# Kernel tuning notes

Hardware: AMD Instinct MI355X
Metric: run time of the kernel (lower is better)

Reference implementation:

```python
import jax, jax.numpy as jnp
import numpy as np

T_DATA = 20000
E_NO = 2000
I_NO = 500
SUB = 12
T_SYN = 200
T_HIST = 100
SB = 3   # syn_basis_no
HB = 3   # hist_basis_no
PB = 3   # prop_basis_no


def setup_inputs() -> dict:
    key = jax.random.key(0)
    ks = jax.random.split(key, 20)
    f32 = jnp.float32
    S_e = (jax.random.uniform(ks[0], (T_DATA, E_NO)) < 0.05).astype(f32)
    S_i = (jax.random.uniform(ks[1], (T_DATA, I_NO)) < 0.05).astype(f32)
    C_syn_e = (jax.random.uniform(ks[2], (SUB, E_NO)) < 1.0 / SUB).astype(f32)
    C_syn_i = (jax.random.uniform(ks[3], (SUB, I_NO)) < 1.0 / SUB).astype(f32)
    # dendritic adjacency: strictly lower-triangular-ish sparse connectivity
    C_den = (jax.random.uniform(ks[4], (SUB, SUB)) < 0.15).astype(f32) * jnp.tril(jnp.ones((SUB, SUB), f32), -1)
    return {
        'S_e': S_e, 'S_i': S_i,
        'C_syn_e': C_syn_e, 'C_syn_i': C_syn_i, 'C_den': C_den,
        'W_s_syn': jax.random.normal(ks[5], (SUB, SB, 2), f32) * 0.04,
        'W_ns_syn': jax.random.normal(ks[6], (SUB, SB, 2), f32) * 0.02,
        'Delta_s_syn': jax.random.uniform(ks[7], (SUB, 2), f32),
        'Delta_ns_syn': jax.random.uniform(ks[8], (SUB, 2), f32),
        'Theta_s': jnp.zeros((SUB,), f32),
        'Theta_ns': jnp.zeros((SUB,), f32),
        'W_s_sub': jax.random.uniform(ks[9], (SUB,), f32),
        'W_ns_sub': jax.random.uniform(ks[10], (SUB,), f32),
        'W_s_hist': jax.random.uniform(ks[11], (SUB - 1, HB), f32) * -0.04,
        'W_ns_hist': jax.random.uniform(ks[12], (SUB - 1, HB), f32) * -0.02,
        'W_s_prop': jax.random.uniform(ks[13], (SUB, PB), f32) * 0.04,
        'W_ns_prop': jax.random.uniform(ks[14], (SUB, PB), f32) * 0.02,
    }


def _syn_kernels(W, Delta):
    # W: [sub, SB, 2], Delta: [sub, 2] -> kern [sub, 2, T_SYN]
    t = jnp.arange(T_SYN, dtype=jnp.float32)
    ts = jnp.maximum(t[None, None, :] - jnp.exp(Delta)[:, :, None], 0.0)  # [sub,2,T]
    tau = jnp.exp(jnp.arange(SB, dtype=jnp.float32) * 0.5)                # Tau = arange(0, SB*0.5, 0.5)
    tt = ts[:, None, :, :] / tau[None, :, None, None]                     # [sub,SB,2,T]
    return jnp.einsum('sbct,sbc->sct', tt * jnp.exp(-tt), W)


def _decay_kernels(W, T, nb):
    # W: [n, nb] -> kern [n, T]; tau_b = exp(0.5*b)
    t = jnp.arange(T, dtype=jnp.float32)
    tau = jnp.exp(jnp.arange(nb, dtype=jnp.float32) * 0.5)
    tt = t[None, :] / tau[:, None]  # [nb, T]
    return jnp.einsum('bt,sb->st', tt * jnp.exp(-tt), W)


def _causal_conv(x, kern):
    # x: [T, C], kern: [C, K]; out[t, c] = sum_k kern[c, k] * x[t-k, c]
    C, K = kern.shape
    y = jax.lax.conv_general_dilated(
        x.T[None], kern[:, None, ::-1], (1,), [(K - 1, 0)],
        feature_group_count=C, dimension_numbers=('NCW', 'OIW', 'NCW'))
    return y[0].T


def reference(S_e, S_i, C_syn_e, C_syn_i, C_den, W_s_syn, W_ns_syn,
              Delta_s_syn, Delta_ns_syn, Theta_s, Theta_ns,
              W_s_sub, W_ns_sub, W_s_hist, W_ns_hist, W_s_prop, W_ns_prop):
    sub = C_den.shape[0]
    # --- synaptic kernels + causal filtering (vectorized over subunits) ---
    k_s = _syn_kernels(W_s_syn, Delta_s_syn)      # [sub,2,T_SYN]
    k_ns = _syn_kernels(W_ns_syn, Delta_ns_syn)
    IN_e = S_e @ C_syn_e.T                        # [T, sub]
    IN_i = S_i @ C_syn_i.T
    syn_s_in = _causal_conv(IN_e, k_s[:, 0]) + _causal_conv(IN_i, k_s[:, 1])    # [T, sub]
    syn_ns_in = _causal_conv(IN_e, k_ns[:, 0]) + _causal_conv(IN_i, k_ns[:, 1])
    # --- history / propagation kernels ---
    hist_s = _decay_kernels(W_s_hist, T_HIST, HB)   # [sub-1, T_HIST]
    hist_ns = _decay_kernels(W_ns_hist, T_HIST, HB)
    prop_s = _decay_kernels(W_s_prop, T_HIST, PB)   # [sub, T_HIST]
    prop_ns = _decay_kernels(W_ns_prop, T_HIST, PB)
    # Z_pad (spike history buffer) stays zero in this forward, so the filtered
    # hist/prop terms are identically zero; keep the computation for fidelity.
    z0 = jnp.zeros((sub - 1, T_HIST), syn_s_in.dtype)
    filt_s_hist = (hist_s * z0).sum(-1)      # [sub-1]
    filt_ns_hist = (hist_ns * z0).sum(-1)
    sp0 = C_den[:, 1:] @ z0                   # [sub, T_HIST]
    filt_s_prop = (prop_s * sp0).sum(-1)      # [sub]
    filt_ns_prop = (prop_ns * sp0).sum(-1)

    def step(carry, syn_t):
        Y_s, Y_ns = carry
        s_t, ns_t = syn_t
        X_s = s_t + filt_s_prop + C_den @ Y_s + Theta_s
        X_s = X_s.at[1:].add(filt_s_hist)
        X_ns = ns_t + filt_ns_prop + C_den @ Y_ns + Theta_ns
        X_ns = X_ns.at[1:].add(filt_ns_hist)
        X_ns_out = jax.nn.sigmoid(X_ns)
        Y_ns_n = X_ns_out * W_ns_sub
        sig_s = jax.nn.sigmoid(X_s)
        Y_s_n = jnp.concatenate([sig_s[:1] * W_s_sub[:1], X_ns_out[1:] * W_s_sub[1:]])
        # per-step output: [Y_s(t+1), Y_ns(t+1), spike probs of non-root subunits]
        return (Y_s_n, Y_ns_n), jnp.concatenate([Y_s_n, Y_ns_n, sig_s[1:]])

    init = (jnp.zeros((sub,), syn_s_in.dtype), jnp.zeros((sub,), syn_s_in.dtype))
    _, out = jax.lax.scan(step, init, (syn_s_in, syn_ns_in))
    return out  # [T_DATA, 3*sub - 1]


if __name__ == '__main__':
    inp = setup_inputs()
    o = reference(**inp)
    print(o.shape)
```

## Files before the change

### kernel.cpp

```cpp
#include <hip/hip_runtime.h>

typedef unsigned int uint;
typedef unsigned long long u64;

#define TD 20000
#define WS_H      0
#define WS_SPREAD 9600
#define WS_IN     14600
#define WS_SYN    494600

__device__ __forceinline__ float sigf(float x) { return 1.f / (1.f + __expf(-x)); }

__global__ __launch_bounds__(256) void k1_precomp(
    const float* __restrict__ Ce, const float* __restrict__ Ci,
    const float* __restrict__ Wsy_s, const float* __restrict__ Wsy_ns,
    const float* __restrict__ Del_s, const float* __restrict__ Del_ns,
    float* __restrict__ ws) {
  int p = blockIdx.x * 256 + threadIdx.x;
  if (p < 2400) {
    int k = p / 12, s = p - (p / 12) * 12;
    float o[4];
    for (int ch = 0; ch < 2; ++ch) {
      const float* W = ch ? Wsy_ns : Wsy_s;
      const float* D = ch ? Del_ns : Del_s;
      for (int c = 0; c < 2; ++c) {
        float ts = fmaxf((float)k - __expf(D[s * 2 + c]), 0.f);
        float v = 0.f;
        for (int b = 0; b < 3; ++b) {
          float tt = ts * __expf(-0.5f * (float)b);
          v += W[s * 6 + b * 2 + c] * tt * __expf(-tt);
        }
        o[ch * 2 + c] = v;
      }
    }
    float* H = ws + WS_H + (size_t)(k * 12 + s) * 4;
    H[0] = o[0]; H[1] = o[1]; H[2] = o[2]; H[3] = o[3];
  }
  int q = p - 2400;
  if (q >= 0 && q < 2500) {
    uint m = 0;
    if (q < 2000) {
      for (int s = 0; s < 12; ++s) m |= (Ce[s * 2000 + q] != 0.f ? (1u << s) : 0u);
    } else {
      int e = q - 2000;
      for (int s = 0; s < 12; ++s) m |= (Ci[s * 500 + e] != 0.f ? (1u << s) : 0u);
    }
    u64 sp = 0ull;
    for (int s = 0; s < 12; ++s) sp |= (u64)((m >> s) & 1u) << (5 * s);
    ((uint2*)(ws + WS_SPREAD))[q] = make_uint2((uint)sp, (uint)(sp >> 32));
  }
}

__global__ __launch_bounds__(256) void k2_project(
    const float* __restrict__ Se, const float* __restrict__ Si,
    float* __restrict__ ws) {
  __shared__ __align__(16) uint2 sp[2500];
  {
    const uint2* g = (const uint2*)(ws + WS_SPREAD);
    for (int p = threadIdx.x; p < 2500; p += 256) sp[p] = g[p];
  }
  __syncthreads();
  const int lane = threadIdx.x & 63;
  const int t = blockIdx.x * 4 + (threadIdx.x >> 6);
  const uint4* SP4 = (const uint4*)sp;
  float* INb = ws + WS_IN;

  uint eTot[12];
#pragma unroll
  for (int s = 0; s < 12; ++s) eTot[s] = 0u;
  u64 acc = 0ull;
  const float4* Sr = (const float4*)(Se + (size_t)t * 2000);
#pragma unroll
  for (int it = 0; it < 8; ++it) {
    int i4 = lane + it * 64;
    if (i4 < 500) {
      float4 sv = Sr[i4];
      uint4 a = SP4[2 * i4];
      uint4 b = SP4[2 * i4 + 1];
      u64 m0 = (u64)a.x | ((u64)a.y << 32);
      u64 m1 = (u64)a.z | ((u64)a.w << 32);
      u64 m2 = (u64)b.x | ((u64)b.y << 32);
      u64 m3 = (u64)b.z | ((u64)b.w << 32);
      acc += (sv.x != 0.f ? m0 : 0ull);
      acc += (sv.y != 0.f ? m1 : 0ull);
      acc += (sv.z != 0.f ? m2 : 0ull);
      acc += (sv.w != 0.f ? m3 : 0ull);
    }
    if (it == 3) {
#pragma unroll
      for (int s = 0; s < 12; ++s) eTot[s] += (uint)(acc >> (5 * s)) & 31u;
      acc = 0ull;
    }
  }
#pragma unroll
  for (int s = 0; s < 12; ++s) eTot[s] += (uint)(acc >> (5 * s)) & 31u;
  u64 accI = 0ull;
  const float4* Sir = (const float4*)(Si + (size_t)t * 500);
#pragma unroll
  for (int it = 0; it < 2; ++it) {
    int i4 = lane + it * 64;
    if (i4 < 125) {
      float4 sv = Sir[i4];
      uint4 a = SP4[1000 + 2 * i4];
      uint4 b = SP4[1000 + 2 * i4 + 1];
      u64 m0 = (u64)a.x | ((u64)a.y << 32);
      u64 m1 = (u64)a.z | ((u64)a.w << 32);
      u64 m2 = (u64)b.x | ((u64)b.y << 32);
      u64 m3 = (u64)b.z | ((u64)b.w << 32);
      accI += (sv.x != 0.f ? m0 : 0ull);
      accI += (sv.y != 0.f ? m1 : 0ull);
      accI += (sv.z != 0.f ? m2 : 0ull);
      accI += (sv.w != 0.f ? m3 : 0ull);
    }
  }
  uint pk[12];
#pragma unroll
  for (int s = 0; s < 12; ++s)
    pk[s] = eTot[s] | (((uint)(accI >> (5 * s)) & 31u) << 16);
#pragma unroll
  for (int s = 0; s < 12; ++s) {
    uint v = pk[s];
    v += __shfl_xor(v, 32, 64);
    v += __shfl_xor(v, 16, 64);
    v += __shfl_xor(v, 8, 64);
    v += __shfl_xor(v, 4, 64);
    v += __shfl_xor(v, 2, 64);
    v += __shfl_xor(v, 1, 64);
    pk[s] = v;
  }
  if (lane == 0) {
    float4* o = (float4*)(INb + (size_t)t * 24);
    o[0] = make_float4((float)(pk[0] & 0xffffu), (float)(pk[1] & 0xffffu),
                       (float)(pk[2] & 0xffffu), (float)(pk[3] & 0xffffu));
    o[1] = make_float4((float)(pk[4] & 0xffffu), (float)(pk[5] & 0xffffu),
                       (float)(pk[6] & 0xffffu), (float)(pk[7] & 0xffffu));
    o[2] = make_float4((float)(pk[8] & 0xffffu), (float)(pk[9] & 0xffffu),
                       (float)(pk[10] & 0xffffu), (float)(pk[11] & 0xffffu));
    o[3] = make_float4((float)(pk[0] >> 16), (float)(pk[1] >> 16),
                       (float)(pk[2] >> 16), (float)(pk[3] >> 16));
    o[4] = make_float4((float)(pk[4] >> 16), (float)(pk[5] >> 16),
                       (float)(pk[6] >> 16), (float)(pk[7] >> 16));
    o[5] = make_float4((float)(pk[8] >> 16), (float)(pk[9] >> 16),
                       (float)(pk[10] >> 16), (float)(pk[11] >> 16));
  }
}

__global__ __launch_bounds__(256) void k3_conv(float* __restrict__ ws) {
  __shared__ float tile[6 * 264];
  __shared__ float red[4 * 64 * 7];
  const int g = blockIdx.y;
  const int t0 = blockIdx.x * 64;
  const float* INb = ws + WS_IN;
  for (int p = threadIdx.x; p < 263 * 6; p += 256) {
    int row = p / 6, c = p - row * 6;
    int ch = (c < 3) ? (3 * g + c) : (9 + 3 * g + c);
    int gt = t0 - 199 + row;
    tile[c * 264 + row] = (gt >= 0 && gt < TD) ? INb[(size_t)gt * 24 + ch] : 0.f;
  }
  __syncthreads();
  const int lane = threadIdx.x & 63;
  const int q = threadIdx.x >> 6;
  const float4* H4 = (const float4*)(ws + WS_H);
  float accs[3] = {0.f, 0.f, 0.f}, accn[3] = {0.f, 0.f, 0.f};
  for (int kk = 0; kk < 25; ++kk) {
    int k = q * 50 + kk * 2;
    int rb = lane + 198 - k;
#pragma unroll
    for (int s = 0; s < 3; ++s) {
      float ve0 = tile[s * 264 + rb];
      float ve1 = tile[s * 264 + rb + 1];
      float vi0 = tile[(3 + s) * 264 + rb];
      float vi1 = tile[(3 + s) * 264 + rb + 1];
      float4 h0 = H4[k * 12 + 3 * g + s];
      float4 h1 = H4[(k + 1) * 12 + 3 * g + s];
      accs[s] += h0.x * ve1 + h0.y * vi1 + h1.x * ve0 + h1.y * vi0;
      accn[s] += h0.z * ve1 + h0.w * vi1 + h1.z * ve0 + h1.w * vi0;
    }
  }
  float* mr = red + (q * 64 + lane) * 7;
#pragma unroll
  for (int s = 0; s < 3; ++s) { mr[s] = accs[s]; mr[3 + s] = accn[s]; }
  __syncthreads();
  for (int p = threadIdx.x; p < 64 * 6; p += 256) {
    int row = p / 6, c = p - row * 6;
    if (t0 + row < TD) {
      float sum = red[row * 7 + c] + red[(64 + row) * 7 + c] +
                  red[(128 + row) * 7 + c] + red[(192 + row) * 7 + c];
      int ch = (c < 3) ? (3 * g + c) : (9 + 3 * g + c);
      ws[WS_SYN + (size_t)(t0 + row) * 24 + ch] = sum;
    }
  }
}

__global__ void k45_out(
    const float* __restrict__ Cden, const float* __restrict__ Ws_sub,
    const float* __restrict__ Wns_sub, const float* __restrict__ Th_s,
    const float* __restrict__ Th_ns, const float* __restrict__ ws,
    float* __restrict__ out) {
  __shared__ float lout[64 * 35];
  const int t = blockIdx.x * 64 + threadIdx.x;
  float v[35];
#pragma unroll
  for (int m = 0; m < 35; ++m) v[m] = 0.f;
  if (t < TD) {
    const float* SYN = ws + WS_SYN;
    float dns[12][12];
#pragma unroll
    for (int i = 1; i < 12; ++i)
#pragma unroll
      for (int j = 0; j < i; ++j) dns[i][j] = Cden[i * 12 + j] * Wns_sub[j];
    float th[12];
#pragma unroll
    for (int i = 0; i < 12; ++i) th[i] = Th_ns[i];
    float ap[12], an[12];
#pragma unroll
    for (int i = 0; i < 12; ++i) { ap[i] = 0.f; an[i] = 0.f; }
    int start = t - 12; if (start < 0) start = 0;
    for (int tau = start; tau <= t; ++tau) {
      const float4* sr = (const float4*)(SYN + (size_t)tau * 24 + 12);
      float4 s0 = sr[0], s1 = sr[1], s2 = sr[2];
      float sn[12] = {s0.x, s0.y, s0.z, s0.w, s1.x, s1.y, s1.z, s1.w,
                      s2.x, s2.y, s2.z, s2.w};
#pragma unroll
      for (int i = 0; i < 12; ++i) {
        float x = sn[i] + th[i];
#pragma unroll
        for (int j = 0; j < i; ++j) x += dns[i][j] * ap[j];
        an[i] = sigf(x);
      }
      if (tau < t) {
#pragma unroll
        for (int i = 0; i < 12; ++i) ap[i] = an[i];
      }
    }
    float sns[12];
    {
      const float4* sr = (const float4*)(SYN + (size_t)t * 24);
      float4 s0 = sr[0], s1 = sr[1], s2 = sr[2];
      sns[0] = s0.x; sns[1] = s0.y; sns[2] = s0.z; sns[3] = s0.w;
      sns[4] = s1.x; sns[5] = s1.y; sns[6] = s1.z; sns[7] = s1.w;
      sns[8] = s2.x; sns[9] = s2.y; sns[10] = s2.z; sns[11] = s2.w;
    }
    float carry[12];
    carry[0] = (t > 0) ? Ws_sub[0] * sigf(SYN[(size_t)(t - 1) * 24] + Th_s[0]) : 0.f;
#pragma unroll
    for (int j = 1; j < 12; ++j) carry[j] = Ws_sub[j] * ap[j];
    float B[12];
#pragma unroll
    for (int i = 0; i < 12; ++i) {
      float x = sns[i] + Th_s[i];
#pragma unroll
      for (int j = 0; j < i; ++j) x += Cden[i * 12 + j] * carry[j];
      B[i] = sigf(x);
    }
    v[0] = B[0] * Ws_sub[0];
#pragma unroll
    for (int i = 1; i < 12; ++i) v[i] = an[i] * Ws_sub[i];
#pragma unroll
    for (int i = 0; i < 12; ++i) v[12 + i] = an[i] * Wns_sub[i];
#pragma unroll
    for (int i = 1; i < 12; ++i) v[23 + i] = B[i];
  }
#pragma unroll
  for (int m = 0; m < 35; ++m) lout[threadIdx.x * 35 + m] = v[m];
  __syncthreads();
  const int t0 = blockIdx.x * 64;
  int nrow = TD - t0; if (nrow > 64) nrow = 64;
  const int valid = nrow * 35;
  for (int p = threadIdx.x; p < valid; p += 64) out[(size_t)t0 * 35 + p] = lout[p];
}

extern "C" void kernel_launch(void* const* d_in, const int* in_sizes, int n_in,
                              void* d_out, int out_size, void* d_ws, size_t ws_size,
                              hipStream_t stream) {
  const float* Se = (const float*)d_in[0];
  const float* Si = (const float*)d_in[1];
  const float* Ce = (const float*)d_in[2];
  const float* Ci = (const float*)d_in[3];
  const float* Cden = (const float*)d_in[4];
  const float* Wsy_s = (const float*)d_in[5];
  const float* Wsy_ns = (const float*)d_in[6];
  const float* Del_s = (const float*)d_in[7];
  const float* Del_ns = (const float*)d_in[8];
  const float* Th_s = (const float*)d_in[9];
  const float* Th_ns = (const float*)d_in[10];
  const float* Ws_sub = (const float*)d_in[11];
  const float* Wns_sub = (const float*)d_in[12];
  float* ws = (float*)d_ws;
  float* out = (float*)d_out;

  k1_precomp<<<20, 256, 0, stream>>>(Ce, Ci, Wsy_s, Wsy_ns, Del_s, Del_ns, ws);
  k2_project<<<5000, 256, 0, stream>>>(Se, Si, ws);
  dim3 g3(313, 4);
  k3_conv<<<g3, 256, 0, stream>>>(ws);
  k45_out<<<313, 64, 0, stream>>>(Cden, Ws_sub, Wns_sub, Th_s, Th_ns, ws, out);
}
```

Before: 327.0 us.

## Map four timesteps per wave in projection kernel, drop LDS staging, use DPP reductions

The projection kernel now has each 16-lane row of a wave process its own timestep instead of one whole wave per timestep. The grid shrinks to a quarter of the blocks, and the shared-memory copy of the spread masks is removed in favour of reading them straight from global memory, which should be L1/L2 resident. The cross-lane reduction uses DPP row_shr adds within 16 lanes instead of 64-lane shuffles. Per-lane work grows, which may reduce memory parallelism per lane. Global mask reads could also cost more than LDS reads.

```diff
diff --git a/kernel.cpp b/kernel.cpp
--- a/kernel.cpp
+++ b/kernel.cpp
@@ -10,6 +10,15 @@
 #define WS_SYN    494600
 
 __device__ __forceinline__ float sigf(float x) { return 1.f / (1.f + __expf(-x)); }
+
+__device__ __forceinline__ uint dpp_shr_add(uint v, const int ctrl_is ) {
+  switch (ctrl_is) {
+    case 1: return v + (uint)__builtin_amdgcn_update_dpp(0, (int)v, 0x111, 0xf, 0xf, true);
+    case 2: return v + (uint)__builtin_amdgcn_update_dpp(0, (int)v, 0x112, 0xf, 0xf, true);
+    case 4: return v + (uint)__builtin_amdgcn_update_dpp(0, (int)v, 0x114, 0xf, 0xf, true);
+    default: return v + (uint)__builtin_amdgcn_update_dpp(0, (int)v, 0x118, 0xf, 0xf, true);
+  }
+}
 
 __global__ __launch_bounds__(256) void k1_precomp(
     const float* __restrict__ Ce, const float* __restrict__ Ci,
@@ -54,15 +63,12 @@
 __global__ __launch_bounds__(256) void k2_project(
     const float* __restrict__ Se, const float* __restrict__ Si,
     float* __restrict__ ws) {
-  __shared__ __align__(16) uint2 sp[2500];
-  {
-    const uint2* g = (const uint2*)(ws + WS_SPREAD);
-    for (int p = threadIdx.x; p < 2500; p += 256) sp[p] = g[p];
-  }
-  __syncthreads();
   const int lane = threadIdx.x & 63;
-  const int t = blockIdx.x * 4 + (threadIdx.x >> 6);
-  const uint4* SP4 = (const uint4*)sp;
+  const int wv = blockIdx.x * 4 + (threadIdx.x >> 6);
+  const int r = lane >> 4;
+  const int c = lane & 15;
+  const int t = wv * 4 + r;
+  const uint4* SP4 = (const uint4*)(ws + WS_SPREAD);
   float* INb = ws + WS_IN;
 
   uint eTot[12];
@@ -71,8 +77,8 @@
   u64 acc = 0ull;
   const float4* Sr = (const float4*)(Se + (size_t)t * 2000);
 #pragma unroll
-  for (int it = 0; it < 8; ++it) {
-    int i4 = lane + it * 64;
+  for (int it = 0; it < 32; ++it) {
+    int i4 = c + it * 16;
     if (i4 < 500) {
       float4 sv = Sr[i4];
       uint4 a = SP4[2 * i4];
@@ -86,19 +92,20 @@
       acc += (sv.z != 0.f ? m2 : 0ull);
       acc += (sv.w != 0.f ? m3 : 0ull);
     }
-    if (it == 3) {
+    if ((it & 3) == 3) {
 #pragma unroll
       for (int s = 0; s < 12; ++s) eTot[s] += (uint)(acc >> (5 * s)) & 31u;
       acc = 0ull;
     }
   }
-#pragma unroll
-  for (int s = 0; s < 12; ++s) eTot[s] += (uint)(acc >> (5 * s)) & 31u;
+  uint iTot[12];
+#pragma unroll
+  for (int s = 0; s < 12; ++s) iTot[s] = 0u;
   u64 accI = 0ull;
   const float4* Sir = (const float4*)(Si + (size_t)t * 500);
 #pragma unroll
-  for (int it = 0; it < 2; ++it) {
-    int i4 = lane + it * 64;
+  for (int it = 0; it < 8; ++it) {
+    int i4 = c + it * 16;
     if (i4 < 125) {
       float4 sv = Sir[i4];
       uint4 a = SP4[1000 + 2 * i4];
@@ -112,23 +119,28 @@
       accI += (sv.z != 0.f ? m2 : 0ull);
       accI += (sv.w != 0.f ? m3 : 0ull);
     }
-  }
+    if (it == 3) {
+#pragma unroll
+      for (int s = 0; s < 12; ++s) iTot[s] += (uint)(accI >> (5 * s)) & 31u;
+      accI = 0ull;
+    }
+  }
+#pragma unroll
+  for (int s = 0; s < 12; ++s) iTot[s] += (uint)(accI >> (5 * s)) & 31u;
+
   uint pk[12];
 #pragma unroll
-  for (int s = 0; s < 12; ++s)
-    pk[s] = eTot[s] | (((uint)(accI >> (5 * s)) & 31u) << 16);
+  for (int s = 0; s < 12; ++s) pk[s] = eTot[s] | (iTot[s] << 16);
 #pragma unroll
   for (int s = 0; s < 12; ++s) {
     uint v = pk[s];
-    v += __shfl_xor(v, 32, 64);
-    v += __shfl_xor(v, 16, 64);
-    v += __shfl_xor(v, 8, 64);
-    v += __shfl_xor(v, 4, 64);
-    v += __shfl_xor(v, 2, 64);
-    v += __shfl_xor(v, 1, 64);
+    v = dpp_shr_add(v, 1);
+    v = dpp_shr_add(v, 2);
+    v = dpp_shr_add(v, 4);
+    v = dpp_shr_add(v, 8);
     pk[s] = v;
   }
-  if (lane == 0) {
+  if (c == 15) {
     float4* o = (float4*)(INb + (size_t)t * 24);
     o[0] = make_float4((float)(pk[0] & 0xffffu), (float)(pk[1] & 0xffffu),
                        (float)(pk[2] & 0xffffu), (float)(pk[3] & 0xffffu));
@@ -290,7 +302,7 @@
   float* out = (float*)d_out;
 
   k1_precomp<<<20, 256, 0, stream>>>(Ce, Ci, Wsy_s, Wsy_ns, Del_s, Del_ns, ws);
-  k2_project<<<5000, 256, 0, stream>>>(Se, Si, ws);
+  k2_project<<<1250, 256, 0, stream>>>(Se, Si, ws);
   dim3 g3(313, 4);
   k3_conv<<<g3, 256, 0, stream>>>(ws);
   k45_out<<<313, 64, 0, stream>>>(Cden, Ws_sub, Wns_sub, Th_s, Th_ns, ws, out);
```

Result: slower. 342.2 us (+4.6%).
